# Kernel optimization log

Measured on AMD Instinct MI355X. Metric: run time of the kernel, lower is better.

The kernel has to match this reference:

```python
import jax, jax.numpy as jnp
import numpy as np

B, T, D = 512, 512, 128   # batch, time_step, input_dim (soft-label classes)
EMB = 32                  # embedding_size
UNITS = 32                # rnn_utils
L = 2                     # rnn_layer_num
ND = 2                    # dense_num - 1 hidden denses
NC = 11                   # output classes
EPS = 1e-3                # keras BatchNormalization default epsilon


def _gru_step(h, x_t, W, U, b):
    # Keras GRUCell, reset_after=True, gate order [z, r, h], recurrent_activation=sigmoid, activation=relu
    gi = x_t @ W + b[0]            # (B, 3U) input projection + input bias
    gr = h @ U + b[1]              # (B, 3U) recurrent projection + recurrent bias
    iz, ir, ih = jnp.split(gi, 3, axis=-1)
    rz, rr, rh = jnp.split(gr, 3, axis=-1)
    z = jax.nn.sigmoid(iz + rz)
    r = jax.nn.sigmoid(ir + rr)
    hh = jax.nn.relu(ih + r * rh)
    return z * h + (1.0 - z) * hh


def _run_gru(xs, W, U, b):
    # xs: (S, B, F) -> outputs (S, B, UNITS), zero initial state
    h0 = jnp.zeros((xs.shape[1], U.shape[0]), xs.dtype)
    def step(h, x_t):
        h2 = _gru_step(h, x_t, W, U, b)
        return h2, h2
    _, ys = jax.lax.scan(step, h0, xs)
    return ys


def setup_inputs() -> dict:
    key = jax.random.key(0)
    ks = jax.random.split(key, 12)
    s = 0.1
    return {
        "x": jax.random.normal(ks[0], (B, T, D), jnp.float32),
        "emb": jax.random.normal(ks[1], (D, EMB), jnp.float32) * s,
        "Wl": jax.random.normal(ks[2], (L, EMB, 3 * UNITS), jnp.float32) * s,
        "Ul": jax.random.normal(ks[3], (L, UNITS, 3 * UNITS), jnp.float32) * s,
        "bl": jnp.zeros((L, 2, 3 * UNITS), jnp.float32),
        "Wr": jax.random.normal(ks[4], (L, EMB, 3 * UNITS), jnp.float32) * s,
        "Ur": jax.random.normal(ks[5], (L, UNITS, 3 * UNITS), jnp.float32) * s,
        "br": jnp.zeros((L, 2, 3 * UNITS), jnp.float32),
        "bn_gamma": jnp.ones((L, UNITS), jnp.float32),
        "bn_beta": jnp.zeros((L, UNITS), jnp.float32),
        "Wd": jax.random.normal(ks[6], (ND, UNITS, 32), jnp.float32) * s,
        "bd": jnp.zeros((ND, 32), jnp.float32),
        "dbn_gamma": jnp.ones((ND, 32), jnp.float32),
        "dbn_beta": jnp.zeros((ND, 32), jnp.float32),
        "Wf": jax.random.normal(ks[7], (32, NC), jnp.float32) * s,
        "bf": jnp.zeros((NC,), jnp.float32),
    }


def reference(x, emb, Wl, Ul, bl, Wr, Ur, br, bn_gamma, bn_beta,
              Wd, bd, dbn_gamma, dbn_beta, Wf, bf):
    Bsz = x.shape[0]
    idx = jnp.argmax(x, axis=2)             # (B, T) hard labels
    h = emb[idx]                            # (B, T, EMB)
    ht = jnp.transpose(h, (1, 0, 2))        # (T, B, EMB) time-major
    for i in range(L):
        # left GRU consumes items 1..T-1; outputs_left[0] is None (-> zero)
        left = _run_gru(ht[1:], Wl[i], Ul[i], bl[i])             # (T-1, B, U), time t covers items 1..t
        # right GRU consumes items T-2..0 in reverse; outputs_right at time T-1 is None (-> zero)
        right = _run_gru(ht[:-1][::-1], Wr[i], Ur[i], br[i])     # step k is time T-2-k
        zero = jnp.zeros((1, Bsz, UNITS), ht.dtype)
        merged = (jnp.concatenate([zero, left], axis=0)
                  + jnp.concatenate([right[::-1], zero], axis=0))  # (T, B, U)
        # keras BatchNormalization (training): stats over batch AND time, axis=-1
        m = merged.mean(axis=(0, 1))
        v = merged.var(axis=(0, 1))
        ht = bn_gamma[i] * (merged - m) * jax.lax.rsqrt(v + EPS) + bn_beta[i]
    xd = jnp.transpose(ht, (1, 0, 2))       # (B, T, U)
    out = xd
    for j in range(ND):
        # faithful to source bug: every dense reads the layer-stack output `item`, only the last survives
        o = jax.nn.relu(xd @ Wd[j] + bd[j])                     # (B, T, 32)
        # per-time-step BN (original loops over time): stats over batch dim only
        m = o.mean(axis=0, keepdims=True)
        v = o.var(axis=0, keepdims=True)
        out = dbn_gamma[j] * (o - m) * jax.lax.rsqrt(v + EPS) + dbn_beta[j]
    return jax.nn.softmax(out @ Wf + bf, axis=-1)               # (B, T, 11)
```

## Files before the change

kernel.cpp:

```cpp
#include <hip/hip_runtime.h>


#define Bsz 512
#define Tsz 512

typedef unsigned uintv2 __attribute__((ext_vector_type(2)));
typedef _Float16 half8 __attribute__((ext_vector_type(8)));
typedef float f32x4 __attribute__((ext_vector_type(4)));

union H8 { unsigned u[4]; half8 h; };

__device__ __forceinline__ float sigmoid_f(float x) {
    return __builtin_amdgcn_rcpf(1.0f + __expf(-x));
}

__device__ __forceinline__ uintv2 p16(unsigned a, unsigned b) {
#if __has_builtin(__builtin_amdgcn_permlane16_swap)
    return __builtin_amdgcn_permlane16_swap(a, b, false, false);
#else
    asm("v_permlane16_swap_b32 %0, %1" : "+v"(a), "+v"(b));
    uintv2 r; r.x = a; r.y = b; return r;
#endif
}
__device__ __forceinline__ uintv2 p32(unsigned a, unsigned b) {
#if __has_builtin(__builtin_amdgcn_permlane32_swap)
    return __builtin_amdgcn_permlane32_swap(a, b, false, false);
#else
    asm("v_permlane32_swap_b32 %0, %1" : "+v"(a), "+v"(b));
    uintv2 r; r.x = a; r.y = b; return r;
#endif
}

__device__ __forceinline__ void route4(unsigned P0, unsigned P1, unsigned P2, unsigned P3,
                                       unsigned& W0, unsigned& W1, unsigned& W2, unsigned& W3)
{
    uintv2 m = p32(P0, P2);
    uintv2 a = p16(m.x, m.y);
    uintv2 n = p32(P1, P3);
    uintv2 c = p16(n.x, n.y);
    W0 = a.x; W2 = a.y; W1 = c.x; W3 = c.y;
}

__device__ __forceinline__ unsigned pk16(float a, float b) {
    auto h = __builtin_amdgcn_cvt_pkrtz(a, b);
    return __builtin_bit_cast(unsigned, h);
}

__device__ __forceinline__ H8 make_B(float v0, float v1, float v2, float v3,
                                     float v4, float v5, float v6, float v7)
{
    unsigned P0 = pk16(v0, v1), P1 = pk16(v2, v3);
    unsigned P2 = pk16(v4, v5), P3 = pk16(v6, v7);
    H8 b;
    route4(P0, P1, P2, P3, b.u[0], b.u[1], b.u[2], b.u[3]);
    return b;
}

__device__ __forceinline__ void calib_slots(int lane, int cs[8]) {
    unsigned q = (unsigned)(lane >> 4) & 3u;
    unsigned c0 = 4u * q, c1 = 16u + 4u * q;
    unsigned P0 = c0 | ((c0 + 1u) << 16);
    unsigned P1 = (c0 + 2u) | ((c0 + 3u) << 16);
    unsigned P2 = c1 | ((c1 + 1u) << 16);
    unsigned P3 = (c1 + 2u) | ((c1 + 3u) << 16);
    unsigned W0, W1, W2, W3;
    route4(P0, P1, P2, P3, W0, W1, W2, W3);
    cs[0] = W0 & 0xffff; cs[1] = W0 >> 16;
    cs[2] = W1 & 0xffff; cs[3] = W1 >> 16;
    cs[4] = W2 & 0xffff; cs[5] = W2 >> 16;
    cs[6] = W3 & 0xffff; cs[7] = W3 >> 16;
}

__device__ __forceinline__ H8 load_A(const float* __restrict__ M, const int cs[8], int gcol) {
    H8 a;
#pragma unroll
    for (int e = 0; e < 4; ++e)
        a.u[e] = pk16(M[cs[2 * e] * 96 + gcol], M[cs[2 * e + 1] * 96 + gcol]);
    return a;
}

__device__ __forceinline__ f32x4 mfma16(const H8& a, const H8& b, f32x4 c) {
    return __builtin_amdgcn_mfma_f32_16x16x32_f16(a.h, b.h, c, 0, 0, 0);
}

__device__ __forceinline__ float gate1(float az, float ar, float ah, float ai, float h) {
    float z = sigmoid_f(az);
    float r = sigmoid_f(ar);
    float hh = fmaxf(0.f, fmaf(r, ah, ai));
    return hh + z * (h - hh);
}

__global__ __launch_bounds__(256) void lspd_argmax(const float* __restrict__ x, int* __restrict__ idxT)
{
    int wv = threadIdx.x >> 6, lane = threadIdx.x & 63;
    long p = (long)blockIdx.x * 4 + wv;
    const float* xp = x + p * 128;
    float v0 = xp[lane];      int i0 = lane;
    float v1 = xp[64 + lane]; int i1 = 64 + lane;
    if (v1 > v0) { v0 = v1; i0 = i1; }
#pragma unroll
    for (int d = 1; d < 64; d <<= 1) {
        float ov = __shfl_xor(v0, d, 64);
        int   oi = __shfl_xor(i0, d, 64);
        if (ov > v0 || (ov == v0 && oi < i0)) { v0 = ov; i0 = oi; }
    }
    if (lane == 0) idxT[p] = i0;
}

__global__ __launch_bounds__(256) void lspd_tab(
    const float* __restrict__ emb, const float* __restrict__ Wl, const float* __restrict__ bl,
    const float* __restrict__ Wr, const float* __restrict__ br,
    float* __restrict__ tabL, float* __restrict__ tabR)
{
    int flat = blockIdx.x * 256 + threadIdx.x;
    int dir = flat / 12288;
    int r = flat % 12288;
    int i = r / 96, g = r % 96;
    const float* W  = dir ? Wr : Wl;
    const float* bb = dir ? br : bl;
    float acc = bb[g];
#pragma unroll
    for (int k = 0; k < 32; ++k) acc = fmaf(emb[i * 32 + k], W[k * 96 + g], acc);
    (dir ? tabR : tabL)[r] = acc;
}

__global__ __launch_bounds__(64)
__attribute__((amdgpu_waves_per_eu(1, 1)))
void lspd_gru0(
    const int* __restrict__ idxT, const float* __restrict__ tabL, const float* __restrict__ tabR,
    const float* __restrict__ Ul, const float* __restrict__ Ur,
    const float* __restrict__ bl, const float* __restrict__ br,
    float* __restrict__ Lout, float* __restrict__ Rout)
{
    int bid = blockIdx.x;
    int dir = bid >> 5;
    int bg  = bid & 31;
    int lane = threadIdx.x;
    int rl = lane & 15;
    int q  = lane >> 4;
    int b  = bg * 16 + rl;
    const float* U    = dir ? Ur : Ul;
    const float* tab  = dir ? tabR : tabL;
    const float* brec = (dir ? br : bl) + 96;
    float* out        = dir ? Rout : Lout;

    int cs[8];
    calib_slots(lane, cs);

    H8 AUz0 = load_A(U, cs, 0  + rl), AUz1 = load_A(U, cs, 16 + rl);
    H8 AUr0 = load_A(U, cs, 32 + rl), AUr1 = load_A(U, cs, 48 + rl);
    H8 AUh0 = load_A(U, cs, 64 + rl), AUh1 = load_A(U, cs, 80 + rl);
    f32x4 BZ0 = *(const f32x4*)(brec + 0  + 4 * q);
    f32x4 BZ1 = *(const f32x4*)(brec + 16 + 4 * q);
    f32x4 BR0 = *(const f32x4*)(brec + 32 + 4 * q);
    f32x4 BR1 = *(const f32x4*)(brec + 48 + 4 * q);
    f32x4 BH0 = *(const f32x4*)(brec + 64 + 4 * q);
    f32x4 BH1 = *(const f32x4*)(brec + 80 + 4 * q);

    const int* idxrow = idxT + (long)b * Tsz;

#define TT0(s) (dir ? (Tsz - 2 - (s)) : (1 + (s)))
    {
        long zb = ((long)(dir ? Tsz - 1 : 0) * Bsz + b) * 32;
        float4 z4 = make_float4(0.f, 0.f, 0.f, 0.f);
        *(float4*)(out + zb + 4 * q) = z4;
        *(float4*)(out + zb + 16 + 4 * q) = z4;
    }
    long ob = ((long)TT0(0) * Bsz + b) * 32;
    long ostride = (long)(dir ? -1 : 1) * Bsz * 32;

    float4 G0z0, G0z1, G0r0, G0r1, G0h0, G0h1;
    float4 G1z0, G1z1, G1r0, G1r1, G1h0, G1h1;
    float4 G2z0, G2z1, G2r0, G2r1, G2h0, G2h1;
    float4 G3z0, G3z1, G3r0, G3r1, G3h0, G3h1;
#define GFILL(P, TA)                                                           \
    {                                                                          \
        long ta_ = (long)(TA) * 96;                                            \
        P##z0 = *(const float4*)(tab + ta_ + 0  + 4 * q);                      \
        P##z1 = *(const float4*)(tab + ta_ + 16 + 4 * q);                      \
        P##r0 = *(const float4*)(tab + ta_ + 32 + 4 * q);                      \
        P##r1 = *(const float4*)(tab + ta_ + 48 + 4 * q);                      \
        P##h0 = *(const float4*)(tab + ta_ + 64 + 4 * q);                      \
        P##h1 = *(const float4*)(tab + ta_ + 80 + 4 * q);                      \
    }
    GFILL(G0, idxrow[TT0(0)]);
    GFILL(G1, idxrow[TT0(1)]);
    GFILL(G2, idxrow[TT0(2)]);
    GFILL(G3, idxrow[TT0(3)]);
    int i0 = idxrow[TT0(4)];
    int i1 = idxrow[TT0(5)];
    int i2 = idxrow[TT0(6)];
    int i3 = idxrow[TT0(7)];

    float h0 = 0.f, h1 = 0.f, h2 = 0.f, h3 = 0.f, h4 = 0.f, h5 = 0.f, h6 = 0.f, h7 = 0.f;

#define STEP0(Gz0, Gz1, Gr0, Gr1, Gh0, Gh1, IREG, SINEXT)                      \
    {                                                                          \
        H8 Bh = make_B(h0, h1, h2, h3, h4, h5, h6, h7);                        \
        f32x4 Cz0 = mfma16(AUz0, Bh, BZ0);                                     \
        f32x4 Cz1 = mfma16(AUz1, Bh, BZ1);                                     \
        f32x4 Cr0 = mfma16(AUr0, Bh, BR0);                                     \
        f32x4 Cr1 = mfma16(AUr1, Bh, BR1);                                     \
        f32x4 Ch0 = mfma16(AUh0, Bh, BH0);                                     \
        f32x4 Ch1 = mfma16(AUh1, Bh, BH1);                                     \
        h0 = gate1(Cz0.x + Gz0.x, Cr0.x + Gr0.x, Ch0.x, Gh0.x, h0);            \
        h1 = gate1(Cz0.y + Gz0.y, Cr0.y + Gr0.y, Ch0.y, Gh0.y, h1);            \
        h2 = gate1(Cz0.z + Gz0.z, Cr0.z + Gr0.z, Ch0.z, Gh0.z, h2);            \
        h3 = gate1(Cz0.w + Gz0.w, Cr0.w + Gr0.w, Ch0.w, Gh0.w, h3);            \
        h4 = gate1(Cz1.x + Gz1.x, Cr1.x + Gr1.x, Ch1.x, Gh1.x, h4);            \
        h5 = gate1(Cz1.y + Gz1.y, Cr1.y + Gr1.y, Ch1.y, Gh1.y, h5);            \
        h6 = gate1(Cz1.z + Gz1.z, Cr1.z + Gr1.z, Ch1.z, Gh1.z, h6);            \
        h7 = gate1(Cz1.w + Gz1.w, Cr1.w + Gr1.w, Ch1.w, Gh1.w, h7);            \
        *(float4*)(out + ob + 4 * q) = make_float4(h0, h1, h2, h3);            \
        *(float4*)(out + ob + 16 + 4 * q) = make_float4(h4, h5, h6, h7);       \
        ob += ostride;                                                         \
        long tb2 = (long)IREG * 96;                                            \
        Gz0 = *(const float4*)(tab + tb2 + 0  + 4 * q);                        \
        Gz1 = *(const float4*)(tab + tb2 + 16 + 4 * q);                        \
        Gr0 = *(const float4*)(tab + tb2 + 32 + 4 * q);                        \
        Gr1 = *(const float4*)(tab + tb2 + 48 + 4 * q);                        \
        Gh0 = *(const float4*)(tab + tb2 + 64 + 4 * q);                        \
        Gh1 = *(const float4*)(tab + tb2 + 80 + 4 * q);                        \
        int sn = (SINEXT); if (sn > Tsz - 2) sn = Tsz - 2;                     \
        IREG = idxrow[TT0(sn)];                                                \
    }

    for (int sb = 0; sb < 508; sb += 4) {
        STEP0(G0z0, G0z1, G0r0, G0r1, G0h0, G0h1, i0, sb + 8);
        STEP0(G1z0, G1z1, G1r0, G1r1, G1h0, G1h1, i1, sb + 9);
        STEP0(G2z0, G2z1, G2r0, G2r1, G2h0, G2h1, i2, sb + 10);
        STEP0(G3z0, G3z1, G3r0, G3r1, G3h0, G3h1, i3, sb + 11);
    }
    STEP0(G0z0, G0z1, G0r0, G0r1, G0h0, G0h1, i0, 510);
    STEP0(G1z0, G1z1, G1r0, G1r1, G1h0, G1h1, i1, 510);
    STEP0(G2z0, G2z1, G2r0, G2r1, G2h0, G2h1, i2, 510);
#undef STEP0
#undef GFILL
#undef TT0
}

__global__ __launch_bounds__(256) void lspd_stats(
    const float* __restrict__ A, const float* __restrict__ Bv, float* __restrict__ part)
{
    __shared__ float sS[256], sQ[256];
    int tid = threadIdx.x;
    size_t base = (size_t)blockIdx.x * 65536 + tid;
    float s = 0.f, q = 0.f;
    for (int i = 0; i < 256; ++i) {
        size_t ix = base + (size_t)i * 256;
        float v = A[ix] + Bv[ix];
        s += v; q = fmaf(v, v, q);
    }
    sS[tid] = s; sQ[tid] = q;
    __syncthreads();
    if (tid < 32) {
        float S = 0.f, Q = 0.f;
        for (int j = 0; j < 8; ++j) { S += sS[tid + 32 * j]; Q += sQ[tid + 32 * j]; }
        part[blockIdx.x * 64 + tid] = S;
        part[blockIdx.x * 64 + 32 + tid] = Q;
    }
}

__global__ __launch_bounds__(256) void lspd_fold1(
    const float* __restrict__ part, const float* __restrict__ g0, const float* __restrict__ be0,
    const float* __restrict__ Wl, const float* __restrict__ Wr,
    const float* __restrict__ bl, const float* __restrict__ br,
    float* __restrict__ WpL, float* __restrict__ WpR,
    float* __restrict__ b4L, float* __restrict__ b4R)
{
    __shared__ float sc[32], tc[32];
    int tid = threadIdx.x;
    if (tid < 32) {
        float S = 0.f, Q = 0.f;
        for (int p = 0; p < 128; ++p) { S += part[p * 64 + tid]; Q += part[p * 64 + 32 + tid]; }
        const float invN = 1.0f / 262144.0f;
        float m = S * invN;
        float v = Q * invN - m * m;
        float s = g0[tid] * __builtin_amdgcn_rsqf(v + 1e-3f);
        sc[tid] = s; tc[tid] = be0[tid] - s * m;
    }
    __syncthreads();
    for (int idx = tid; idx < 6144; idx += 256) {
        int dir = idx / 3072, e = idx % 3072, k = e / 96, g = e % 96;
        const float* W1 = (dir ? Wr : Wl) + 3072;
        (dir ? WpR : WpL)[e] = sc[k] * W1[k * 96 + g];
    }
    {
        int idx = tid;
        int dir = idx >> 7, slot = idx & 127, sub = slot >> 5, cc = slot & 31;
        const float* bb = (dir ? br : bl) + 192;
        const float* W1 = (dir ? Wr : Wl) + 3072;
        float r;
        if (sub == 2) {
            r = bb[96 + 64 + cc];
        } else {
            int g = (sub == 3) ? (64 + cc) : (sub * 32 + cc);
            float acc = bb[g];
            for (int k = 0; k < 32; ++k) acc = fmaf(tc[k], W1[k * 96 + g], acc);
            if (sub < 2) acc += bb[96 + g];
            r = acc;
        }
        (dir ? b4R : b4L)[slot] = r;
    }
}

__global__ __launch_bounds__(64)
__attribute__((amdgpu_waves_per_eu(1, 1)))
void lspd_gru1(
    const float* __restrict__ L0, const float* __restrict__ R0,
    const float* __restrict__ WpL, const float* __restrict__ WpR,
    const float* __restrict__ b4L, const float* __restrict__ b4R,
    const float* __restrict__ Ul1, const float* __restrict__ Ur1,
    float* __restrict__ Lout, float* __restrict__ Rout)
{
    int bid = blockIdx.x;
    int dir = bid >> 5;
    int bg  = bid & 31;
    int lane = threadIdx.x;
    int rl = lane & 15;
    int q  = lane >> 4;
    int b  = bg * 16 + rl;
    const float* U  = dir ? Ur1 : Ul1;
    const float* Wp = dir ? WpR : WpL;
    const float* b4 = dir ? b4R : b4L;
    float* out      = dir ? Rout : Lout;

    int cs[8];
    calib_slots(lane, cs);

    H8 AWz0 = load_A(Wp, cs, 0  + rl), AWz1 = load_A(Wp, cs, 16 + rl);
    H8 AWr0 = load_A(Wp, cs, 32 + rl), AWr1 = load_A(Wp, cs, 48 + rl);
    H8 AWh0 = load_A(Wp, cs, 64 + rl), AWh1 = load_A(Wp, cs, 80 + rl);
    H8 AUz0 = load_A(U, cs, 0  + rl),  AUz1 = load_A(U, cs, 16 + rl);
    H8 AUr0 = load_A(U, cs, 32 + rl),  AUr1 = load_A(U, cs, 48 + rl);
    H8 AUh0 = load_A(U, cs, 64 + rl),  AUh1 = load_A(U, cs, 80 + rl);
    f32x4 BZ0 = *(const f32x4*)(b4 + 0   + 4 * q);
    f32x4 BZ1 = *(const f32x4*)(b4 + 16  + 4 * q);
    f32x4 BR0 = *(const f32x4*)(b4 + 32  + 4 * q);
    f32x4 BR1 = *(const f32x4*)(b4 + 48  + 4 * q);
    f32x4 BH0 = *(const f32x4*)(b4 + 64  + 4 * q);
    f32x4 BH1 = *(const f32x4*)(b4 + 80  + 4 * q);
    f32x4 BI0 = *(const f32x4*)(b4 + 96  + 4 * q);
    f32x4 BI1 = *(const f32x4*)(b4 + 112 + 4 * q);

#define XBASE(s) (((long)(dir ? (Tsz - 2 - (s)) : (1 + (s))) * Bsz + b) * 32)
    {
        long zb = ((long)(dir ? Tsz - 1 : 0) * Bsz + b) * 32;
        float4 z4 = make_float4(0.f, 0.f, 0.f, 0.f);
        *(float4*)(out + zb + 4 * q) = z4;
        *(float4*)(out + zb + 16 + 4 * q) = z4;
    }
    long ob = XBASE(0);
    long ostride = (long)(dir ? -1 : 1) * Bsz * 32;

    f32x4 PAz0, PAz1, PAr0, PAr1, PAi0, PAi1;
    f32x4 PBz0, PBz1, PBr0, PBr1, PBi0, PBi1;
    {
        long n0 = XBASE(0);
        float4 ta = *(const float4*)(L0 + n0 + 4 * q);
        float4 tb = *(const float4*)(L0 + n0 + 16 + 4 * q);
        float4 tc = *(const float4*)(R0 + n0 + 4 * q);
        float4 td = *(const float4*)(R0 + n0 + 16 + 4 * q);
        H8 Bx = make_B(ta.x + tc.x, ta.y + tc.y, ta.z + tc.z, ta.w + tc.w,
                       tb.x + td.x, tb.y + td.y, tb.z + td.z, tb.w + td.w);
        PAz0 = mfma16(AWz0, Bx, BZ0);
        PAz1 = mfma16(AWz1, Bx, BZ1);
        PAr0 = mfma16(AWr0, Bx, BR0);
        PAr1 = mfma16(AWr1, Bx, BR1);
        PAi0 = mfma16(AWh0, Bx, BI0);
        PAi1 = mfma16(AWh1, Bx, BI1);
    }
    float4 la0, lb0, ra0, rb0, la1, lb1, ra1, rb1;
    float4 la2, lb2, ra2, rb2, la3, lb3, ra3, rb3;
    {
        long n1 = XBASE(1);
        la0 = *(const float4*)(L0 + n1 + 4 * q); lb0 = *(const float4*)(L0 + n1 + 16 + 4 * q);
        ra0 = *(const float4*)(R0 + n1 + 4 * q); rb0 = *(const float4*)(R0 + n1 + 16 + 4 * q);
        long n2 = XBASE(2);
        la1 = *(const float4*)(L0 + n2 + 4 * q); lb1 = *(const float4*)(L0 + n2 + 16 + 4 * q);
        ra1 = *(const float4*)(R0 + n2 + 4 * q); rb1 = *(const float4*)(R0 + n2 + 16 + 4 * q);
        long n3 = XBASE(3);
        la2 = *(const float4*)(L0 + n3 + 4 * q); lb2 = *(const float4*)(L0 + n3 + 16 + 4 * q);
        ra2 = *(const float4*)(R0 + n3 + 4 * q); rb2 = *(const float4*)(R0 + n3 + 16 + 4 * q);
        long n4 = XBASE(4);
        la3 = *(const float4*)(L0 + n4 + 4 * q); lb3 = *(const float4*)(L0 + n4 + 16 + 4 * q);
        ra3 = *(const float4*)(R0 + n4 + 4 * q); rb3 = *(const float4*)(R0 + n4 + 16 + 4 * q);
    }
    float h0 = 0.f, h1 = 0.f, h2 = 0.f, h3 = 0.f, h4 = 0.f, h5 = 0.f, h6 = 0.f, h7 = 0.f;

#define STEP1(XLA, XLB, XRA, XRB, Pz0, Pz1, Pr0, Pr1, Pi0, Pi1,                \
              Qz0, Qz1, Qr0, Qr1, Qi0, Qi1, SNEXT)                             \
    {                                                                          \
        H8 Bh = make_B(h0, h1, h2, h3, h4, h5, h6, h7);                        \
        f32x4 Cz0 = mfma16(AUz0, Bh, Pz0);                                     \
        f32x4 Cz1 = mfma16(AUz1, Bh, Pz1);                                     \
        f32x4 Cr0 = mfma16(AUr0, Bh, Pr0);                                     \
        f32x4 Cr1 = mfma16(AUr1, Bh, Pr1);                                     \
        f32x4 Ch0 = mfma16(AUh0, Bh, BH0);                                     \
        f32x4 Ch1 = mfma16(AUh1, Bh, BH1);                                     \
        H8 Bx = make_B(XLA.x + XRA.x, XLA.y + XRA.y, XLA.z + XRA.z,            \
                       XLA.w + XRA.w, XLB.x + XRB.x, XLB.y + XRB.y,            \
                       XLB.z + XRB.z, XLB.w + XRB.w);                          \
        Qz0 = mfma16(AWz0, Bx, BZ0);                                           \
        Qz1 = mfma16(AWz1, Bx, BZ1);                                           \
        Qr0 = mfma16(AWr0, Bx, BR0);                                           \
        Qr1 = mfma16(AWr1, Bx, BR1);                                           \
        Qi0 = mfma16(AWh0, Bx, BI0);                                           \
        Qi1 = mfma16(AWh1, Bx, BI1);                                           \
        int sn = (SNEXT); if (sn > Tsz - 2) sn = Tsz - 2;                      \
        long nb = XBASE(sn);                                                   \
        XLA = *(const float4*)(L0 + nb + 4 * q);                               \
        XLB = *(const float4*)(L0 + nb + 16 + 4 * q);                          \
        XRA = *(const float4*)(R0 + nb + 4 * q);                               \
        XRB = *(const float4*)(R0 + nb + 16 + 4 * q);                          \
        h0 = gate1(Cz0.x, Cr0.x, Ch0.x, Pi0.x, h0);                            \
        h1 = gate1(Cz0.y, Cr0.y, Ch0.y, Pi0.y, h1);                            \
        h2 = gate1(Cz0.z, Cr0.z, Ch0.z, Pi0.z, h2);                            \
        h3 = gate1(Cz0.w, Cr0.w, Ch0.w, Pi0.w, h3);                            \
        h4 = gate1(Cz1.x, Cr1.x, Ch1.x, Pi1.x, h4);                            \
        h5 = gate1(Cz1.y, Cr1.y, Ch1.y, Pi1.y, h5);                            \
        h6 = gate1(Cz1.z, Cr1.z, Ch1.z, Pi1.z, h6);                            \
        h7 = gate1(Cz1.w, Cr1.w, Ch1.w, Pi1.w, h7);                            \
        *(float4*)(out + ob + 4 * q) = make_float4(h0, h1, h2, h3);            \
        *(float4*)(out + ob + 16 + 4 * q) = make_float4(h4, h5, h6, h7);       \
        ob += ostride;                                                         \
    }

    for (int sb = 0; sb < 508; sb += 4) {
        STEP1(la0, lb0, ra0, rb0,
              PAz0, PAz1, PAr0, PAr1, PAi0, PAi1,
              PBz0, PBz1, PBr0, PBr1, PBi0, PBi1, sb + 5);
        STEP1(la1, lb1, ra1, rb1,
              PBz0, PBz1, PBr0, PBr1, PBi0, PBi1,
              PAz0, PAz1, PAr0, PAr1, PAi0, PAi1, sb + 6);
        STEP1(la2, lb2, ra2, rb2,
              PAz0, PAz1, PAr0, PAr1, PAi0, PAi1,
              PBz0, PBz1, PBr0, PBr1, PBi0, PBi1, sb + 7);
        STEP1(la3, lb3, ra3, rb3,
              PBz0, PBz1, PBr0, PBr1, PBi0, PBi1,
              PAz0, PAz1, PAr0, PAr1, PAi0, PAi1, sb + 8);
    }
    STEP1(la0, lb0, ra0, rb0,
          PAz0, PAz1, PAr0, PAr1, PAi0, PAi1,
          PBz0, PBz1, PBr0, PBr1, PBi0, PBi1, 510);
    STEP1(la1, lb1, ra1, rb1,
          PBz0, PBz1, PBr0, PBr1, PBi0, PBi1,
          PAz0, PAz1, PAr0, PAr1, PAi0, PAi1, 510);
    STEP1(la2, lb2, ra2, rb2,
          PAz0, PAz1, PAr0, PAr1, PAi0, PAi1,
          PBz0, PBz1, PBr0, PBr1, PBi0, PBi1, 510);
#undef STEP1
#undef XBASE
}

__global__ __launch_bounds__(256) void lspd_fold2(
    const float* __restrict__ part, const float* __restrict__ g1, const float* __restrict__ be1,
    const float* __restrict__ Wd1, const float* __restrict__ bd1,
    float* __restrict__ Wdp, float* __restrict__ bdp)
{
    __shared__ float sc[32], tc[32];
    int tid = threadIdx.x;
    if (tid < 32) {
        float S = 0.f, Q = 0.f;
        for (int p = 0; p < 128; ++p) { S += part[p * 64 + tid]; Q += part[p * 64 + 32 + tid]; }
        const float invN = 1.0f / 262144.0f;
        float m = S * invN;
        float v = Q * invN - m * m;
        float s = g1[tid] * __builtin_amdgcn_rsqf(v + 1e-3f);
        sc[tid] = s; tc[tid] = be1[tid] - s * m;
    }
    __syncthreads();
    for (int idx = tid; idx < 1024; idx += 256) {
        int k = idx >> 5;
        Wdp[idx] = sc[k] * Wd1[idx];
    }
    if (tid < 32) {
        float acc = bd1[tid];
        for (int k = 0; k < 32; ++k) acc = fmaf(tc[k], Wd1[k * 32 + tid], acc);
        bdp[tid] = acc;
    }
}

__global__ __launch_bounds__(512) void lspd_final(
    const float* __restrict__ L1a, const float* __restrict__ R1a,
    const float* __restrict__ Wdp, const float* __restrict__ bdp,
    const float* __restrict__ dg, const float* __restrict__ db,
    const float* __restrict__ Wf, const float* __restrict__ bfv,
    float* __restrict__ outp)
{
    __shared__ alignas(16) float sW[1024];
    __shared__ float sb[32], sWf[352], sbf[16], sS[32], sT[32];
    __shared__ float redS[8][32], redQ[8][32];
    int tid = threadIdx.x, t = blockIdx.x;
    for (int i = tid; i < 1024; i += 512) sW[i] = Wdp[i];
    if (tid < 32)  sb[tid] = bdp[tid];
    if (tid < 352) sWf[tid] = Wf[tid];
    if (tid < 11)  sbf[tid] = bfv[tid];
    __syncthreads();

    size_t base = ((size_t)t * Bsz + tid) * 32;
    float xv[32];
#pragma unroll
    for (int c2 = 0; c2 < 32; c2 += 4) {
        float4 a = *(const float4*)(L1a + base + c2);
        float4 b = *(const float4*)(R1a + base + c2);
        xv[c2 + 0] = a.x + b.x; xv[c2 + 1] = a.y + b.y;
        xv[c2 + 2] = a.z + b.z; xv[c2 + 3] = a.w + b.w;
    }
    float o[32];
#pragma unroll
    for (int g = 0; g < 32; ++g) o[g] = sb[g];
#pragma unroll
    for (int k = 0; k < 32; ++k) {
        float xk = xv[k];
#pragma unroll
        for (int g4 = 0; g4 < 8; ++g4) {
            float4 w = *(const float4*)(sW + k * 32 + g4 * 4);
            o[g4 * 4 + 0] = fmaf(xk, w.x, o[g4 * 4 + 0]);
            o[g4 * 4 + 1] = fmaf(xk, w.y, o[g4 * 4 + 1]);
            o[g4 * 4 + 2] = fmaf(xk, w.z, o[g4 * 4 + 2]);
            o[g4 * 4 + 3] = fmaf(xk, w.w, o[g4 * 4 + 3]);
        }
    }
#pragma unroll
    for (int g = 0; g < 32; ++g) o[g] = fmaxf(o[g], 0.f);

    int wv = tid >> 6, lane = tid & 63;
    for (int g = 0; g < 32; ++g) {
        float s = o[g], q = o[g] * o[g];
        for (int d = 1; d < 64; d <<= 1) {
            s += __shfl_xor(s, d, 64);
            q += __shfl_xor(q, d, 64);
        }
        if (lane == 0) { redS[wv][g] = s; redQ[wv][g] = q; }
    }
    __syncthreads();
    if (tid < 32) {
        float S = 0.f, Q = 0.f;
        for (int w2 = 0; w2 < 8; ++w2) { S += redS[w2][tid]; Q += redQ[w2][tid]; }
        float m = S * (1.0f / 512.0f);
        float v = Q * (1.0f / 512.0f) - m * m;
        float s = dg[tid] * __builtin_amdgcn_rsqf(v + 1e-3f);
        sS[tid] = s; sT[tid] = db[tid] - s * m;
    }
    __syncthreads();

    float lg[11];
#pragma unroll
    for (int n = 0; n < 11; ++n) lg[n] = sbf[n];
#pragma unroll
    for (int g = 0; g < 32; ++g) {
        float no = fmaf(o[g], sS[g], sT[g]);
#pragma unroll
        for (int n = 0; n < 11; ++n) lg[n] = fmaf(no, sWf[g * 11 + n], lg[n]);
    }
    float mx = lg[0];
#pragma unroll
    for (int n = 1; n < 11; ++n) mx = fmaxf(mx, lg[n]);
    float sum = 0.f;
#pragma unroll
    for (int n = 0; n < 11; ++n) { lg[n] = __expf(lg[n] - mx); sum += lg[n]; }
    float inv = __builtin_amdgcn_rcpf(sum);
    float* op = outp + ((size_t)tid * Tsz + t) * 11;
#pragma unroll
    for (int n = 0; n < 11; ++n) op[n] = lg[n] * inv;
}

extern "C" void kernel_launch(void* const* d_in, const int* in_sizes, int n_in,
                              void* d_out, int out_size, void* d_ws, size_t ws_size,
                              hipStream_t stream)
{
    (void)in_sizes; (void)n_in; (void)out_size; (void)ws_size;
    const float* x   = (const float*)d_in[0];
    const float* emb = (const float*)d_in[1];
    const float* Wl  = (const float*)d_in[2];
    const float* Ul  = (const float*)d_in[3];
    const float* bl  = (const float*)d_in[4];
    const float* Wr  = (const float*)d_in[5];
    const float* Ur  = (const float*)d_in[6];
    const float* br  = (const float*)d_in[7];
    const float* bng = (const float*)d_in[8];
    const float* bnb = (const float*)d_in[9];
    const float* Wd  = (const float*)d_in[10];
    const float* bd  = (const float*)d_in[11];
    const float* dg  = (const float*)d_in[12];
    const float* db  = (const float*)d_in[13];
    const float* Wf  = (const float*)d_in[14];
    const float* bf  = (const float*)d_in[15];
    float* out = (float*)d_out;

    float* ws = (float*)d_ws;
    float* L0 = ws;
    float* R0 = L0 + 8388608;
    float* L1 = R0 + 8388608;
    float* R1 = L1 + 8388608;
    float* rest = R1 + 8388608;
    int* idxT   = (int*)rest;
    float* tabL = rest + 262144;
    float* tabR = tabL + 12288;
    float* part1 = tabR + 12288;
    float* part2 = part1 + 8192;
    float* WpL = part2 + 8192;
    float* WpR = WpL + 3072;
    float* b4L = WpR + 3072;
    float* b4R = b4L + 128;
    float* Wdp = b4R + 128;
    float* bdp = Wdp + 1024;

    lspd_argmax<<<65536, 256, 0, stream>>>(x, idxT);
    lspd_tab<<<96, 256, 0, stream>>>(emb, Wl, bl, Wr, br, tabL, tabR);
    lspd_gru0<<<64, 64, 0, stream>>>(idxT, tabL, tabR, Ul, Ur, bl, br, L0, R0);
    lspd_stats<<<128, 256, 0, stream>>>(L0, R0, part1);
    lspd_fold1<<<1, 256, 0, stream>>>(part1, bng, bnb, Wl, Wr, bl, br, WpL, WpR, b4L, b4R);
    lspd_gru1<<<64, 64, 0, stream>>>(L0, R0, WpL, WpR, b4L, b4R, Ul + 3072, Ur + 3072, L1, R1);
    lspd_stats<<<128, 256, 0, stream>>>(L1, R1, part2);
    lspd_fold2<<<1, 256, 0, stream>>>(part2, bng + 32, bnb + 32, Wd + 1024, bd + 32, Wdp, bdp);
    lspd_final<<<512, 512, 0, stream>>>(L1, R1, Wdp, bdp, dg + 32, db + 32, Wf, bf, out);
}
```

Baseline: 737.5 us.

## Run layer-0 GRU with one wave per sequence using fp32 FMA and DPP broadcasts

The layer-0 GRU kernel changes from 64 waves, each handling 16 sequences with fp16 MFMA, to 1024 waves that each handle a single sequence. Within a wave, the two 32-lane halves each take 16 of the hidden inputs. The state is broadcast with permlane swaps and DPP row broadcasts, the partial dot products are fp32 FMAs, and the halves are summed with a permlane32 swap. This spreads the serial recurrence over many more CUs and shortens the per-step latency chain, and it also drops the fp16 rounding of the state. The cost is more total instructions and less work per wave, and the kernel keeps waves_per_eu(1,1) even though it now launches 1024 waves.

```diff
diff --git a/kernel.cpp b/kernel.cpp
--- a/kernel.cpp
+++ b/kernel.cpp
@@ -30,6 +30,34 @@
     uintv2 r; r.x = a; r.y = b; return r;
 #endif
 }
+
+__device__ __forceinline__ void plswap16_f(float& a, float& b) {
+    uintv2 r = p16(__float_as_uint(a), __float_as_uint(b));
+    a = __uint_as_float(r.x);
+    b = __uint_as_float(r.y);
+}
+__device__ __forceinline__ void plswap16_i(int& a, int& b) {
+    uintv2 r = p16((unsigned)a, (unsigned)b);
+    a = (int)r.x;
+    b = (int)r.y;
+}
+__device__ __forceinline__ float xhalfsum(float a) {
+    uintv2 r = p32(__float_as_uint(a), __float_as_uint(a));
+    return __uint_as_float(r.x) + __uint_as_float(r.y);
+}
+
+#define NB_F(d, s, n) d = __int_as_float(__builtin_amdgcn_update_dpp(0, __float_as_int(s), 0x150 + n, 0xF, 0xF, true))
+#define NB_I(d, s, n) d = __builtin_amdgcn_update_dpp(0, (s), 0x150 + n, 0xF, 0xF, true)
+#define BCAST16F(A, S)                                                         \
+    NB_F(A[0], S, 0);  NB_F(A[1], S, 1);  NB_F(A[2], S, 2);  NB_F(A[3], S, 3); \
+    NB_F(A[4], S, 4);  NB_F(A[5], S, 5);  NB_F(A[6], S, 6);  NB_F(A[7], S, 7); \
+    NB_F(A[8], S, 8);  NB_F(A[9], S, 9);  NB_F(A[10], S, 10); NB_F(A[11], S, 11); \
+    NB_F(A[12], S, 12); NB_F(A[13], S, 13); NB_F(A[14], S, 14); NB_F(A[15], S, 15)
+#define BCAST16I(A, S)                                                         \
+    NB_I(A[0], S, 0);  NB_I(A[1], S, 1);  NB_I(A[2], S, 2);  NB_I(A[3], S, 3); \
+    NB_I(A[4], S, 4);  NB_I(A[5], S, 5);  NB_I(A[6], S, 6);  NB_I(A[7], S, 7); \
+    NB_I(A[8], S, 8);  NB_I(A[9], S, 9);  NB_I(A[10], S, 10); NB_I(A[11], S, 11); \
+    NB_I(A[12], S, 12); NB_I(A[13], S, 13); NB_I(A[14], S, 14); NB_I(A[15], S, 15)
 
 __device__ __forceinline__ void route4(unsigned P0, unsigned P1, unsigned P2, unsigned P3,
                                        unsigned& W0, unsigned& W1, unsigned& W2, unsigned& W3)
@@ -132,110 +160,95 @@
     const float* __restrict__ bl, const float* __restrict__ br,
     float* __restrict__ Lout, float* __restrict__ Rout)
 {
-    int bid = blockIdx.x;
-    int dir = bid >> 5;
-    int bg  = bid & 31;
+    int wid = blockIdx.x;
+    int dir = wid >> 9;
+    int b = wid & 511;
     int lane = threadIdx.x;
-    int rl = lane & 15;
-    int q  = lane >> 4;
-    int b  = bg * 16 + rl;
+    int half = lane >> 5, c = lane & 31;
     const float* U    = dir ? Ur : Ul;
     const float* tab  = dir ? tabR : tabL;
     const float* brec = (dir ? br : bl) + 96;
     float* out        = dir ? Rout : Lout;
 
-    int cs[8];
-    calib_slots(lane, cs);
-
-    H8 AUz0 = load_A(U, cs, 0  + rl), AUz1 = load_A(U, cs, 16 + rl);
-    H8 AUr0 = load_A(U, cs, 32 + rl), AUr1 = load_A(U, cs, 48 + rl);
-    H8 AUh0 = load_A(U, cs, 64 + rl), AUh1 = load_A(U, cs, 80 + rl);
-    f32x4 BZ0 = *(const f32x4*)(brec + 0  + 4 * q);
-    f32x4 BZ1 = *(const f32x4*)(brec + 16 + 4 * q);
-    f32x4 BR0 = *(const f32x4*)(brec + 32 + 4 * q);
-    f32x4 BR1 = *(const f32x4*)(brec + 48 + 4 * q);
-    f32x4 BH0 = *(const f32x4*)(brec + 64 + 4 * q);
-    f32x4 BH1 = *(const f32x4*)(brec + 80 + 4 * q);
+    int ksA = c, ksB = c;
+    plswap16_i(ksA, ksB);
+    bool selA = ((ksA >> 4) == half);
+    int ksel = selA ? ksA : ksB;
+    int kk[16];
+    BCAST16I(kk, ksel);
+
+    float u0[16], u1[16], u2[16];
+#pragma unroll
+    for (int j = 0; j < 16; ++j) {
+        u0[j] = U[kk[j] * 96 + c];
+        u1[j] = U[kk[j] * 96 + 32 + c];
+        u2[j] = U[kk[j] * 96 + 64 + c];
+    }
+    float bZ = half ? 0.f : brec[c];
+    float bR = half ? 0.f : brec[32 + c];
+    float bH = half ? 0.f : brec[64 + c];
+#pragma unroll
+    for (int j = 0; j < 16; ++j) {
+        asm volatile("" : "+v"(u0[j]), "+v"(u1[j]), "+v"(u2[j]));
+    }
+    asm volatile("" : "+v"(bZ), "+v"(bR), "+v"(bH));
 
     const int* idxrow = idxT + (long)b * Tsz;
+    if (lane < 32) out[(((long)(dir ? Tsz - 1 : 0)) * Bsz + b) * 32 + c] = 0.f;
 
 #define TT0(s) (dir ? (Tsz - 2 - (s)) : (1 + (s)))
-    {
-        long zb = ((long)(dir ? Tsz - 1 : 0) * Bsz + b) * 32;
-        float4 z4 = make_float4(0.f, 0.f, 0.f, 0.f);
-        *(float4*)(out + zb + 4 * q) = z4;
-        *(float4*)(out + zb + 16 + 4 * q) = z4;
-    }
-    long ob = ((long)TT0(0) * Bsz + b) * 32;
+    long ob = ((long)TT0(0) * Bsz + b) * 32 + c;
     long ostride = (long)(dir ? -1 : 1) * Bsz * 32;
 
-    float4 G0z0, G0z1, G0r0, G0r1, G0h0, G0h1;
-    float4 G1z0, G1z1, G1r0, G1r1, G1h0, G1h1;
-    float4 G2z0, G2z1, G2r0, G2r1, G2h0, G2h1;
-    float4 G3z0, G3z1, G3r0, G3r1, G3h0, G3h1;
-#define GFILL(P, TA)                                                           \
-    {                                                                          \
-        long ta_ = (long)(TA) * 96;                                            \
-        P##z0 = *(const float4*)(tab + ta_ + 0  + 4 * q);                      \
-        P##z1 = *(const float4*)(tab + ta_ + 16 + 4 * q);                      \
-        P##r0 = *(const float4*)(tab + ta_ + 32 + 4 * q);                      \
-        P##r1 = *(const float4*)(tab + ta_ + 48 + 4 * q);                      \
-        P##h0 = *(const float4*)(tab + ta_ + 64 + 4 * q);                      \
-        P##h1 = *(const float4*)(tab + ta_ + 80 + 4 * q);                      \
-    }
-    GFILL(G0, idxrow[TT0(0)]);
-    GFILL(G1, idxrow[TT0(1)]);
-    GFILL(G2, idxrow[TT0(2)]);
-    GFILL(G3, idxrow[TT0(3)]);
+    float g0z, g0r, g0h, g1z, g1r, g1h, g2z, g2r, g2h, g3z, g3r, g3h;
+    { int i = idxrow[TT0(0)]; g0z = tab[i * 96 + c]; g0r = tab[i * 96 + 32 + c]; g0h = tab[i * 96 + 64 + c]; }
+    { int i = idxrow[TT0(1)]; g1z = tab[i * 96 + c]; g1r = tab[i * 96 + 32 + c]; g1h = tab[i * 96 + 64 + c]; }
+    { int i = idxrow[TT0(2)]; g2z = tab[i * 96 + c]; g2r = tab[i * 96 + 32 + c]; g2h = tab[i * 96 + 64 + c]; }
+    { int i = idxrow[TT0(3)]; g3z = tab[i * 96 + c]; g3r = tab[i * 96 + 32 + c]; g3h = tab[i * 96 + 64 + c]; }
     int i0 = idxrow[TT0(4)];
     int i1 = idxrow[TT0(5)];
     int i2 = idxrow[TT0(6)];
     int i3 = idxrow[TT0(7)];
-
-    float h0 = 0.f, h1 = 0.f, h2 = 0.f, h3 = 0.f, h4 = 0.f, h5 = 0.f, h6 = 0.f, h7 = 0.f;
-
-#define STEP0(Gz0, Gz1, Gr0, Gr1, Gh0, Gh1, IREG, SINEXT)                      \
+    float h = 0.f;
+
+#define GSTEP(GZ, GR, GH, IREG, SNEXT)                                         \
     {                                                                          \
-        H8 Bh = make_B(h0, h1, h2, h3, h4, h5, h6, h7);                        \
-        f32x4 Cz0 = mfma16(AUz0, Bh, BZ0);                                     \
-        f32x4 Cz1 = mfma16(AUz1, Bh, BZ1);                                     \
-        f32x4 Cr0 = mfma16(AUr0, Bh, BR0);                                     \
-        f32x4 Cr1 = mfma16(AUr1, Bh, BR1);                                     \
-        f32x4 Ch0 = mfma16(AUh0, Bh, BH0);                                     \
-        f32x4 Ch1 = mfma16(AUh1, Bh, BH1);                                     \
-        h0 = gate1(Cz0.x + Gz0.x, Cr0.x + Gr0.x, Ch0.x, Gh0.x, h0);            \
-        h1 = gate1(Cz0.y + Gz0.y, Cr0.y + Gr0.y, Ch0.y, Gh0.y, h1);            \
-        h2 = gate1(Cz0.z + Gz0.z, Cr0.z + Gr0.z, Ch0.z, Gh0.z, h2);            \
-        h3 = gate1(Cz0.w + Gz0.w, Cr0.w + Gr0.w, Ch0.w, Gh0.w, h3);            \
-        h4 = gate1(Cz1.x + Gz1.x, Cr1.x + Gr1.x, Ch1.x, Gh1.x, h4);            \
-        h5 = gate1(Cz1.y + Gz1.y, Cr1.y + Gr1.y, Ch1.y, Gh1.y, h5);            \
-        h6 = gate1(Cz1.z + Gz1.z, Cr1.z + Gr1.z, Ch1.z, Gh1.z, h6);            \
-        h7 = gate1(Cz1.w + Gz1.w, Cr1.w + Gr1.w, Ch1.w, Gh1.w, h7);            \
-        *(float4*)(out + ob + 4 * q) = make_float4(h0, h1, h2, h3);            \
-        *(float4*)(out + ob + 16 + 4 * q) = make_float4(h4, h5, h6, h7);       \
+        float ha = h, hb = h;                                                  \
+        plswap16_f(ha, hb);                                                    \
+        float hs = selA ? ha : hb;                                             \
+        float hk[16];                                                          \
+        BCAST16F(hk, hs);                                                      \
+        float az = bZ, ar = bR, ah = bH;                                       \
+        _Pragma("unroll")                                                      \
+        for (int n = 0; n < 16; ++n) {                                         \
+            az = fmaf(hk[n], u0[n], az);                                       \
+            ar = fmaf(hk[n], u1[n], ar);                                       \
+            ah = fmaf(hk[n], u2[n], ah);                                       \
+        }                                                                      \
+        az = xhalfsum(az); ar = xhalfsum(ar); ah = xhalfsum(ah);               \
+        float z = sigmoid_f(az + GZ);                                          \
+        float r = sigmoid_f(ar + GR);                                          \
+        float hh = fmaxf(0.f, fmaf(r, ah, GH));                                \
+        h = hh + z * (h - hh);                                                 \
+        if (lane < 32) out[ob] = h;                                            \
         ob += ostride;                                                         \
-        long tb2 = (long)IREG * 96;                                            \
-        Gz0 = *(const float4*)(tab + tb2 + 0  + 4 * q);                        \
-        Gz1 = *(const float4*)(tab + tb2 + 16 + 4 * q);                        \
-        Gr0 = *(const float4*)(tab + tb2 + 32 + 4 * q);                        \
-        Gr1 = *(const float4*)(tab + tb2 + 48 + 4 * q);                        \
-        Gh0 = *(const float4*)(tab + tb2 + 64 + 4 * q);                        \
-        Gh1 = *(const float4*)(tab + tb2 + 80 + 4 * q);                        \
-        int sn = (SINEXT); if (sn > Tsz - 2) sn = Tsz - 2;                     \
+        GZ = tab[IREG * 96 + c];                                               \
+        GR = tab[IREG * 96 + 32 + c];                                          \
+        GH = tab[IREG * 96 + 64 + c];                                          \
+        int sn = (SNEXT); if (sn > Tsz - 2) sn = Tsz - 2;                      \
         IREG = idxrow[TT0(sn)];                                                \
     }
 
     for (int sb = 0; sb < 508; sb += 4) {
-        STEP0(G0z0, G0z1, G0r0, G0r1, G0h0, G0h1, i0, sb + 8);
-        STEP0(G1z0, G1z1, G1r0, G1r1, G1h0, G1h1, i1, sb + 9);
-        STEP0(G2z0, G2z1, G2r0, G2r1, G2h0, G2h1, i2, sb + 10);
-        STEP0(G3z0, G3z1, G3r0, G3r1, G3h0, G3h1, i3, sb + 11);
-    }
-    STEP0(G0z0, G0z1, G0r0, G0r1, G0h0, G0h1, i0, 510);
-    STEP0(G1z0, G1z1, G1r0, G1r1, G1h0, G1h1, i1, 510);
-    STEP0(G2z0, G2z1, G2r0, G2r1, G2h0, G2h1, i2, 510);
-#undef STEP0
-#undef GFILL
+        GSTEP(g0z, g0r, g0h, i0, sb + 8);
+        GSTEP(g1z, g1r, g1h, i1, sb + 9);
+        GSTEP(g2z, g2r, g2h, i2, sb + 10);
+        GSTEP(g3z, g3r, g3h, i3, sb + 11);
+    }
+    GSTEP(g0z, g0r, g0h, i0, 510);
+    GSTEP(g1z, g1r, g1h, i1, 510);
+    GSTEP(g2z, g2r, g2h, i2, 510);
+#undef GSTEP
 #undef TT0
 }
 
@@ -609,7 +622,7 @@
 
     lspd_argmax<<<65536, 256, 0, stream>>>(x, idxT);
     lspd_tab<<<96, 256, 0, stream>>>(emb, Wl, bl, Wr, br, tabL, tabR);
-    lspd_gru0<<<64, 64, 0, stream>>>(idxT, tabL, tabR, Ul, Ur, bl, br, L0, R0);
+    lspd_gru0<<<1024, 64, 0, stream>>>(idxT, tabL, tabR, Ul, Ur, bl, br, L0, R0);
     lspd_stats<<<128, 256, 0, stream>>>(L0, R0, part1);
     lspd_fold1<<<1, 256, 0, stream>>>(part1, bng, bnb, Wl, Wr, bl, br, WpL, WpR, b4L, b4R);
     lspd_gru1<<<64, 64, 0, stream>>>(L0, R0, WpL, WpR, b4L, b4R, Ul + 3072, Ur + 3072, L1, R1);
```

Measured after the change: 673.4 us. 1.1x faster.
